# Kernel tuning notes

Hardware: AMD Instinct MI355X
Metric: run time of the kernel (lower is better)

## Reference

```python
import jax, jax.numpy as jnp
import numpy as np

N_NODES = 50000
N_HEDGES = 20000
N_EDGES = 800000
D = 128
H = 4


def setup_inputs() -> dict:
    key = jax.random.key(0)
    ks = jax.random.split(key, 12)
    s = 1.0 / np.sqrt(D)
    return {
        "x_node": jax.random.normal(ks[0], (N_NODES, D), jnp.float32),
        "x_edge": jax.random.normal(ks[1], (N_HEDGES, D), jnp.float32),
        "src": jax.random.randint(ks[2], (N_EDGES,), 0, N_NODES, jnp.int32),
        "dst": jax.random.randint(ks[3], (N_EDGES,), 0, N_HEDGES, jnp.int32),
        "Wq": jax.random.normal(ks[4], (D, D), jnp.float32) * s,
        "bq": jnp.zeros((D,), jnp.float32),
        "Wk": jax.random.normal(ks[5], (D, D), jnp.float32) * s,
        "bk": jnp.zeros((D,), jnp.float32),
        "Wv": jax.random.normal(ks[6], (D, D), jnp.float32) * s,
        "bv": jnp.zeros((D,), jnp.float32),
        "Wo": jax.random.normal(ks[7], (D, D), jnp.float32) * s,
        "bo": jnp.zeros((D,), jnp.float32),
    }


def reference(x_node, x_edge, src, dst, Wq, bq, Wk, bk, Wv, bv, Wo, bo):
    N = x_node.shape[0]
    hd = Wq.shape[1] // H  # head_dim = 32
    Q = (x_node @ Wq + bq).reshape(N, H, hd)
    K = (x_edge @ Wk + bk).reshape(-1, H, hd)
    V = (x_edge @ Wv + bv).reshape(-1, H, hd)
    # per-edge gather: [E, H, hd]
    Qe = Q[src]
    Ke = K[dst]
    Ve = V[dst]
    # per-edge, per-head scores: [E, H]
    scores = jnp.einsum("ehd,ehd->eh", Qe, Ke) / jnp.sqrt(jnp.float32(hd))
    # segment softmax grouped by src node
    m = jax.ops.segment_max(scores, src, num_segments=N)  # [N, H]
    e = jnp.exp(scores - m[src])
    z = jax.ops.segment_sum(e, src, num_segments=N)  # [N, H]
    w = e / z[src]  # [E, H]
    # weighted scatter-add of V messages back to src nodes
    msg = w[:, :, None] * Ve  # [E, H, hd]
    out = jax.ops.segment_sum(msg, src, num_segments=N)  # [N, H, hd]
    out = out.reshape(N, -1)
    return out @ Wo + bo + x_node
```

## Files before the change

### kernel.cpp

```cpp
#include <hip/hip_runtime.h>

#define D 128
#define STRIDE 6144

typedef _Float16 f16;
typedef f16 f16x2 __attribute__((ext_vector_type(2)));
typedef f16 f16x8 __attribute__((ext_vector_type(8)));
typedef float f32x4 __attribute__((ext_vector_type(4)));

__device__ inline f16x2 u2h(unsigned u) { return __builtin_bit_cast(f16x2, u); }
__device__ inline unsigned h2u(f16x2 h) { return __builtin_bit_cast(unsigned, h); }

__device__ inline float dot2(unsigned a, unsigned b, float c) {
#if __has_builtin(__builtin_amdgcn_fdot2)
    return __builtin_amdgcn_fdot2(u2h(a), u2h(b), c, false);
#else
    f16x2 x = u2h(a), y = u2h(b);
    return c + (float)x.x * (float)y.x + (float)x.y * (float)y.y;
#endif
}

__global__ __launch_bounds__(256) void bucket_split(const int* __restrict__ src,
                                                    const int* __restrict__ dst,
                                                    int* __restrict__ bucket_cnt,
                                                    unsigned* __restrict__ temp, int E) {
    __shared__ int hist[256];
    __shared__ int cur[256];
    int t = threadIdx.x;
    hist[t] = 0;
    __syncthreads();
    int base = blockIdx.x * 4096;
    int lim = E - base; if (lim > 4096) lim = 4096;
    for (int i = t; i < lim; i += 256) atomicAdd(&hist[src[base + i] >> 8], 1);
    __syncthreads();
    int h = hist[t];
    if (h) cur[t] = atomicAdd(&bucket_cnt[t], h);
    __syncthreads();
    for (int i = t; i < lim; i += 256) {
        int s = src[base + i];
        int b = s >> 8;
        int pos = atomicAdd(&cur[b], 1);
        if (pos < STRIDE)
            temp[(size_t)b * STRIDE + pos] = ((unsigned)(s & 255) << 24) | (unsigned)dst[base + i];
    }
}

__global__ void bucket_scan(const int* __restrict__ bucket_cnt, int* __restrict__ boff,
                            int* __restrict__ off, int NBUK, int N, int E) {
    __shared__ int sc[256];
    int t = threadIdx.x;
    int v = (t < NBUK) ? bucket_cnt[t] : 0;
    sc[t] = v;
    __syncthreads();
    for (int d0 = 1; d0 < 256; d0 <<= 1) {
        int u = (t >= d0) ? sc[t - d0] : 0;
        __syncthreads();
        sc[t] += u;
        __syncthreads();
    }
    if (t < NBUK) boff[t] = sc[t] - v;
    if (t == 0) { boff[NBUK] = E; off[N] = E; }
}

__global__ __launch_bounds__(256) void bucket_scatter(const unsigned* __restrict__ temp,
                                                      const int* __restrict__ bucket_cnt,
                                                      const int* __restrict__ boff,
                                                      int* __restrict__ off,
                                                      int* __restrict__ csr_dst, int N) {
    __shared__ int nh[256], cur[256], wsum[4];
    __shared__ int lds_dst[STRIDE];
    int b = blockIdx.x, t = threadIdx.x;
    int cnt = bucket_cnt[b];
    if (cnt > STRIDE) cnt = STRIDE;
    int bo = boff[b];
    const unsigned* tb = temp + (size_t)b * STRIDE;
    nh[t] = 0;
    __syncthreads();
    for (int i = t; i < cnt; i += 256) atomicAdd(&nh[tb[i] >> 24], 1);
    __syncthreads();
    int v = nh[t];
    int inc = v;
#pragma unroll
    for (int m = 1; m < 64; m <<= 1) {
        int u = __shfl_up(inc, m);
        if ((t & 63) >= m) inc += u;
    }
    if ((t & 63) == 63) wsum[t >> 6] = inc;
    __syncthreads();
    int add = 0;
#pragma unroll
    for (int w = 0; w < 4; ++w)
        if (w < (t >> 6)) add += wsum[w];
    int ex = add + inc - v;
    cur[t] = ex;
    int node = (b << 8) + t;
    if (node < N) off[node] = bo + ex;
    __syncthreads();
    for (int i = t; i < cnt; i += 256) {
        unsigned it = tb[i];
        int lpos = atomicAdd(&cur[it >> 24], 1);
        lds_dst[lpos] = (int)(it & 0xFFFFFFu);
    }
    __syncthreads();
    for (int i = t; i < cnt; i += 256) csr_dst[bo + i] = lds_dst[i];
}

__global__ void wt_prep4(const float* __restrict__ W0, const float* __restrict__ W1,
                         const float* __restrict__ W2, const float* __restrict__ W3,
                         f16* __restrict__ Wt) {
    const float* W = (blockIdx.x == 0) ? W0 : (blockIdx.x == 1) ? W1 : (blockIdx.x == 2) ? W2 : W3;
    f16* o = Wt + (size_t)blockIdx.x * D * D;
    int t = threadIdx.x;
#pragma unroll
    for (int i = 0; i < 16; ++i) {
        int f = t + i * 256;
        int k = f >> 5, c4 = f & 31;
        float4 v = *(const float4*)(W + k * D + 4 * c4);
        float vv[4] = {v.x, v.y, v.z, v.w};
#pragma unroll
        for (int e = 0; e < 4; ++e) {
            int c = 4 * c4 + e;
            o[c * D + (((k >> 3) ^ (c & 15)) << 3) + (k & 7)] = (f16)vv[e];
        }
    }
}

__device__ inline void stage_w(const f16* __restrict__ Wt, f16* Wl, int t) {
#pragma unroll
    for (int i = 0; i < 8; ++i) ((uint4*)Wl)[t + i * 256] = ((const uint4*)Wt)[t + i * 256];
}

__device__ inline void stage_x_f32(const float* __restrict__ x, f16* xs, int r0, int nrows, int t) {
#pragma unroll
    for (int i = 0; i < 8; ++i) {
        int f = t + i * 256;
        int r = f >> 5, c4 = f & 31;
        int gr = r0 + r;
        float4 v = {0.f, 0.f, 0.f, 0.f};
        if (gr < nrows) v = *(const float4*)(x + (size_t)gr * D + 4 * c4);
        unsigned lo = h2u((f16x2){(f16)v.x, (f16)v.y});
        unsigned hi = h2u((f16x2){(f16)v.z, (f16)v.w});
        *(uint2*)(xs + r * D + (((c4 >> 1) ^ (r & 15)) << 3) + (c4 & 1) * 4) = (uint2){lo, hi};
    }
}

__device__ inline void mfma_core(const f16* xs, const f16* Wl, f32x4 acc[8], int lane, int w) {
    int lr = lane & 15, g = lane >> 4;
    int arow = 16 * w + lr;
#pragma unroll
    for (int kc = 0; kc < 4; ++kc) {
        int slot = kc * 4 + g;
        f16x8 af = *(const f16x8*)(xs + arow * D + ((slot ^ (arow & 15)) << 3));
#pragma unroll
        for (int ct = 0; ct < 8; ++ct) {
            int col = ct * 16 + lr;
            f16x8 bf = *(const f16x8*)(Wl + col * D + ((slot ^ (col & 15)) << 3));
            acc[ct] = __builtin_amdgcn_mfma_f32_16x16x32_f16(af, bf, acc[ct], 0, 0, 0);
        }
    }
}

__global__ __launch_bounds__(256) void gemm_q(const float* __restrict__ x,
                                              const f16* __restrict__ Wt,
                                              const float* __restrict__ b,
                                              f16* __restrict__ y, int nrows, float oscale) {
    __shared__ __align__(16) f16 Wl[D * D];
    __shared__ __align__(16) f16 xs[64 * D];
    int t = threadIdx.x;
    stage_w(Wt, Wl, t);
    int r0 = blockIdx.x * 64;
    stage_x_f32(x, xs, r0, nrows, t);
    __syncthreads();
    int lane = t & 63, w = t >> 6;
    f32x4 acc[8];
#pragma unroll
    for (int i = 0; i < 8; ++i) acc[i] = (f32x4){0.f, 0.f, 0.f, 0.f};
    mfma_core(xs, Wl, acc, lane, w);
    __syncthreads();
    int lr = lane & 15, g = lane >> 4;
#pragma unroll
    for (int ct = 0; ct < 8; ++ct) {
        int col = ct * 16 + lr;
        float bias = b[col];
#pragma unroll
        for (int rg = 0; rg < 4; ++rg) {
            int row = 16 * w + 4 * g + rg;
            xs[row * D + (((col >> 3) ^ (row & 15)) << 3) + (col & 7)] =
                (f16)((acc[ct][rg] + bias) * oscale);
        }
    }
    __syncthreads();
#pragma unroll
    for (int i = 0; i < 4; ++i) {
        int f = t + i * 256;
        int r = f >> 4, c8 = f & 15;
        if (r0 + r < nrows) {
            uint4 v = *(const uint4*)(xs + r * D + ((c8 ^ (r & 15)) << 3));
            *(uint4*)(y + (size_t)(r0 + r) * D + 8 * c8) = v;
        }
    }
}

__global__ __launch_bounds__(256) void gemm_kv(const float* __restrict__ x,
                                               const f16* __restrict__ WtK,
                                               const f16* __restrict__ WtV,
                                               const float* __restrict__ bk,
                                               const float* __restrict__ bv,
                                               f16* __restrict__ y, int nrows) {
    __shared__ __align__(16) f16 Wl[D * D];
    __shared__ __align__(16) f16 xs[64 * D];
    int t = threadIdx.x;
    int r0 = blockIdx.x * 64;
    stage_w(WtK, Wl, t);
    stage_x_f32(x, xs, r0, nrows, t);
    __syncthreads();
    int lane = t & 63, w = t >> 6;
    f32x4 accK[8], accV[8];
#pragma unroll
    for (int i = 0; i < 8; ++i) accK[i] = accV[i] = (f32x4){0.f, 0.f, 0.f, 0.f};
    mfma_core(xs, Wl, accK, lane, w);
    __syncthreads();
    stage_w(WtV, Wl, t);
    __syncthreads();
    mfma_core(xs, Wl, accV, lane, w);
    __syncthreads();
    int lr = lane & 15, g = lane >> 4;
#pragma unroll
    for (int ct = 0; ct < 8; ++ct) {
        int col = ct * 16 + lr;
        float bbk = bk[col], bbv = bv[col];
        int s = col >> 2, wk = col & 3;
#pragma unroll
        for (int rg = 0; rg < 4; ++rg) {
            int row = 16 * w + 4 * g + rg;
            f16* base = Wl + row * 256 + ((s ^ (row & 15)) << 3);
            base[wk] = (f16)(accK[ct][rg] + bbk);
            base[4 + wk] = (f16)(accV[ct][rg] + bbv);
        }
    }
    __syncthreads();
#pragma unroll
    for (int i = 0; i < 8; ++i) {
        int f = t + i * 256;
        int r = f >> 5, c8 = f & 31;
        if (r0 + r < nrows) {
            uint4 v = *(const uint4*)(Wl + r * 256 + ((c8 ^ (r & 15)) << 3));
            *(uint4*)(y + (size_t)(r0 + r) * 256 + 8 * c8) = v;
        }
    }
}

__global__ __launch_bounds__(256) void gemm_o(const f16* __restrict__ aggh,
                                              const f16* __restrict__ Wt,
                                              const float* __restrict__ b,
                                              const float* __restrict__ resid,
                                              float* __restrict__ y, int nrows) {
    __shared__ __align__(16) f16 Wl[D * D];
    __shared__ __align__(16) f16 xs[64 * D];
    int t = threadIdx.x;
    int r0 = blockIdx.x * 64;
    stage_w(Wt, Wl, t);
#pragma unroll
    for (int i = 0; i < 4; ++i) {
        int f = t + i * 256;
        int r = f >> 4, c8 = f & 15;
        int gr = r0 + r;
        uint4 v = {0u, 0u, 0u, 0u};
        if (gr < nrows) v = *(const uint4*)(aggh + (size_t)gr * D + 8 * c8);
        *(uint4*)(xs + r * D + ((c8 ^ (r & 15)) << 3)) = v;
    }
    __syncthreads();
    int lane = t & 63, w = t >> 6;
    f32x4 acc[8];
#pragma unroll
    for (int i = 0; i < 8; ++i) acc[i] = (f32x4){0.f, 0.f, 0.f, 0.f};
    mfma_core(xs, Wl, acc, lane, w);
    __syncthreads();
    float* Tf = (float*)Wl;
    int lr = lane & 15, g = lane >> 4;
#pragma unroll
    for (int ct = 0; ct < 8; ++ct) {
        int col = ct * 16 + lr;
        float bias = b[col];
        int s = col >> 2, wk = col & 3;
#pragma unroll
        for (int rg = 0; rg < 4; ++rg) {
            int row = 16 * w + 4 * g + rg;
            Tf[row * D + ((s ^ (row & 15)) << 2) + wk] = acc[ct][rg] + bias;
        }
    }
    __syncthreads();
#pragma unroll
    for (int i = 0; i < 8; ++i) {
        int f = t + i * 256;
        int r = f >> 5, c4 = f & 31;
        int gr = r0 + r;
        if (gr < nrows) {
            float4 v = *(const float4*)(Tf + r * D + ((c4 ^ (r & 15)) << 2));
            float4 rv = *(const float4*)(resid + (size_t)gr * D + 4 * c4);
            v.x += rv.x; v.y += rv.y; v.z += rv.z; v.w += rv.w;
            *(float4*)(y + (size_t)gr * D + 4 * c4) = v;
        }
    }
}

__global__ void node_attn3(const f16* __restrict__ Qh, const f16* __restrict__ KVh,
                           const int* __restrict__ off, const int* __restrict__ csr,
                           f16* __restrict__ aggh, int N) {
    int wid = (int)((blockIdx.x * (size_t)blockDim.x + threadIdx.x) >> 6);
    int lane = threadIdx.x & 63;
    if (wid >= N) return;
    int j = lane & 15, g = lane >> 4;
    uint4 qu = *(const uint4*)(Qh + (size_t)wid * D + 8 * j);
    int beg = off[wid], end = off[wid + 1];
    float z = 0.f;
    f16x2 a0 = {0, 0}, a1 = {0, 0}, a2 = {0, 0}, a3 = {0, 0};
    if (beg < end) {
        int pe = beg + g;
        int d = csr[(pe < end) ? pe : end - 1];
        for (int p = beg; p < end; p += 4) {
            int pn = p + 4 + g;
            int dn = csr[(pn < end) ? pn : end - 1];
            bool valid = (p + g) < end;
            const f16* row = KVh + (size_t)d * 256 + 16 * j;
            uint4 kv0 = *(const uint4*)row;
            uint4 kv1 = *(const uint4*)(row + 8);
            float s = dot2(kv1.y, qu.w, dot2(kv1.x, qu.z, dot2(kv0.y, qu.y, dot2(kv0.x, qu.x, 0.f))));
            s += __shfl_xor(s, 1);
            s += __shfl_xor(s, 2);
            float eh = valid ? __expf(s) : 0.f;
            z += eh;
            f16 eh16 = (f16)eh;
            f16x2 e2 = {eh16, eh16};
            a0 += e2 * u2h(kv0.z);
            a1 += e2 * u2h(kv0.w);
            a2 += e2 * u2h(kv1.z);
            a3 += e2 * u2h(kv1.w);
            d = dn;
        }
    }
#pragma unroll
    for (int m = 16; m < 64; m <<= 1) {
        z += __shfl_xor(z, m);
        a0 += u2h(__shfl_xor((int)h2u(a0), m));
        a1 += u2h(__shfl_xor((int)h2u(a1), m));
        a2 += u2h(__shfl_xor((int)h2u(a2), m));
        a3 += u2h(__shfl_xor((int)h2u(a3), m));
    }
    if (g == 0) {
        float inv = (end > beg) ? 1.f / z : 0.f;
        uint4 o;
        o.x = h2u((f16x2){(f16)((float)a0.x * inv), (f16)((float)a0.y * inv)});
        o.y = h2u((f16x2){(f16)((float)a1.x * inv), (f16)((float)a1.y * inv)});
        o.z = h2u((f16x2){(f16)((float)a2.x * inv), (f16)((float)a2.y * inv)});
        o.w = h2u((f16x2){(f16)((float)a3.x * inv), (f16)((float)a3.y * inv)});
        *(uint4*)(aggh + (size_t)wid * D + 8 * j) = o;
    }
}

extern "C" void kernel_launch(void* const* d_in, const int* in_sizes, int n_in,
                              void* d_out, int out_size, void* d_ws, size_t ws_size,
                              hipStream_t stream) {
    const float* x_node = (const float*)d_in[0];
    const float* x_edge = (const float*)d_in[1];
    const int* src = (const int*)d_in[2];
    const int* dst = (const int*)d_in[3];
    const float* Wq = (const float*)d_in[4];
    const float* bq = (const float*)d_in[5];
    const float* Wk = (const float*)d_in[6];
    const float* bk = (const float*)d_in[7];
    const float* Wv = (const float*)d_in[8];
    const float* bv = (const float*)d_in[9];
    const float* Wo = (const float*)d_in[10];
    const float* bo = (const float*)d_in[11];

    int N = in_sizes[0] / D;
    int M = in_sizes[1] / D;
    int E = in_sizes[2];
    int NBUK = (N + 255) >> 8;

    char* p = (char*)d_ws;
    auto alloc = [&](size_t bytes) -> char* {
        char* r = p;
        p += (bytes + 15) & ~(size_t)15;
        return r;
    };
    f16* Wt = (f16*)alloc((size_t)4 * D * D * 2);
    f16* Qh = (f16*)alloc((size_t)N * D * 2);
    f16* KVh = (f16*)alloc((size_t)M * 256 * 2);
    f16* aggh = (f16*)alloc((size_t)N * D * 2);
    int* bucket_cnt = (int*)alloc(256 * 4);
    int* boff = (int*)alloc(257 * 4);
    int* off = (int*)alloc((size_t)(N + 1) * 4);
    unsigned* temp = (unsigned*)alloc((size_t)NBUK * STRIDE * 4);
    int* csr_dst = (int*)alloc((size_t)E * 4);
    float* out = (float*)d_out;

    hipMemsetAsync(bucket_cnt, 0, 256 * 4, stream);

    wt_prep4<<<4, 256, 0, stream>>>(Wq, Wk, Wv, Wo, Wt);

    gemm_q<<<(N + 63) / 64, 256, 0, stream>>>(x_node, Wt, bq, Qh, N, 0.17677669529663687f);
    gemm_kv<<<(M + 63) / 64, 256, 0, stream>>>(x_edge, Wt + D * D, Wt + 2 * D * D, bk, bv, KVh, M);

    bucket_split<<<(E + 4095) / 4096, 256, 0, stream>>>(src, dst, bucket_cnt, temp, E);
    bucket_scan<<<1, 256, 0, stream>>>(bucket_cnt, boff, off, NBUK, N, E);
    bucket_scatter<<<NBUK, 256, 0, stream>>>(temp, bucket_cnt, boff, off, csr_dst, N);

    int ablk = (int)(((size_t)N * 64 + 255) / 256);
    node_attn3<<<ablk, 256, 0, stream>>>(Qh, KVh, off, csr_dst, aggh, N);

    gemm_o<<<(N + 63) / 64, 256, 0, stream>>>(aggh, Wt + 3 * D * D, bo, x_node, out, N);
}
```

Baseline: 133.0 us.

## Process eight edges per wave with software-prefetched KV rows in node attention

The node attention kernel now splits each wave into 8 groups of 8 lanes, so 8 edges are handled per iteration instead of 4, and each lane owns 16 feature dims. The K/V row for the next edge is loaded into registers before the current edge is computed, which is meant to hide gather latency. The head reduction needs one fewer shuffle, the final cross-group reduction needs one more step, and register use roughly doubles. Nodes with about 16 edges on average should waste fewer lanes per iteration.

```diff
diff --git a/kernel.cpp b/kernel.cpp
--- a/kernel.cpp
+++ b/kernel.cpp
@@ -304,57 +304,85 @@
     }
 }
 
-__global__ void node_attn3(const f16* __restrict__ Qh, const f16* __restrict__ KVh,
-                           const int* __restrict__ off, const int* __restrict__ csr,
-                           f16* __restrict__ aggh, int N) {
+__global__ __launch_bounds__(256) void node_attn4(const f16* __restrict__ Qh,
+                                                  const f16* __restrict__ KVh,
+                                                  const int* __restrict__ off,
+                                                  const int* __restrict__ csr,
+                                                  f16* __restrict__ aggh, int N) {
     int wid = (int)((blockIdx.x * (size_t)blockDim.x + threadIdx.x) >> 6);
     int lane = threadIdx.x & 63;
     if (wid >= N) return;
-    int j = lane & 15, g = lane >> 4;
-    uint4 qu = *(const uint4*)(Qh + (size_t)wid * D + 8 * j);
+    int j = lane & 7, g = lane >> 3;
+    const f16* qp = Qh + (size_t)wid * D + 16 * j;
+    uint4 qA = *(const uint4*)qp;
+    uint4 qB = *(const uint4*)(qp + 8);
     int beg = off[wid], end = off[wid + 1];
     float z = 0.f;
     f16x2 a0 = {0, 0}, a1 = {0, 0}, a2 = {0, 0}, a3 = {0, 0};
+    f16x2 a4 = {0, 0}, a5 = {0, 0}, a6 = {0, 0}, a7 = {0, 0};
     if (beg < end) {
         int pe = beg + g;
-        int d = csr[(pe < end) ? pe : end - 1];
-        for (int p = beg; p < end; p += 4) {
-            int pn = p + 4 + g;
+        int d0 = csr[(pe < end) ? pe : end - 1];
+        const f16* r = KVh + (size_t)d0 * 256 + 32 * j;
+        uint4 A0 = *(const uint4*)r;
+        uint4 A1 = *(const uint4*)(r + 8);
+        uint4 A2 = *(const uint4*)(r + 16);
+        uint4 A3 = *(const uint4*)(r + 24);
+        for (int p = beg; p < end; p += 8) {
+            int pn = p + 8 + g;
             int dn = csr[(pn < end) ? pn : end - 1];
+            const f16* rn = KVh + (size_t)dn * 256 + 32 * j;
+            uint4 B0 = *(const uint4*)rn;
+            uint4 B1 = *(const uint4*)(rn + 8);
+            uint4 B2 = *(const uint4*)(rn + 16);
+            uint4 B3 = *(const uint4*)(rn + 24);
             bool valid = (p + g) < end;
-            const f16* row = KVh + (size_t)d * 256 + 16 * j;
-            uint4 kv0 = *(const uint4*)row;
-            uint4 kv1 = *(const uint4*)(row + 8);
-            float s = dot2(kv1.y, qu.w, dot2(kv1.x, qu.z, dot2(kv0.y, qu.y, dot2(kv0.x, qu.x, 0.f))));
+            float s = dot2(A0.x, qA.x, 0.f);
+            s = dot2(A0.y, qA.y, s);
+            s = dot2(A1.x, qA.z, s);
+            s = dot2(A1.y, qA.w, s);
+            s = dot2(A2.x, qB.x, s);
+            s = dot2(A2.y, qB.y, s);
+            s = dot2(A3.x, qB.z, s);
+            s = dot2(A3.y, qB.w, s);
             s += __shfl_xor(s, 1);
-            s += __shfl_xor(s, 2);
             float eh = valid ? __expf(s) : 0.f;
             z += eh;
-            f16 eh16 = (f16)eh;
-            f16x2 e2 = {eh16, eh16};
-            a0 += e2 * u2h(kv0.z);
-            a1 += e2 * u2h(kv0.w);
-            a2 += e2 * u2h(kv1.z);
-            a3 += e2 * u2h(kv1.w);
-            d = dn;
-        }
-    }
-#pragma unroll
-    for (int m = 16; m < 64; m <<= 1) {
+            f16 e16 = (f16)eh;
+            f16x2 e2 = {e16, e16};
+            a0 += e2 * u2h(A0.z); a1 += e2 * u2h(A0.w);
+            a2 += e2 * u2h(A1.z); a3 += e2 * u2h(A1.w);
+            a4 += e2 * u2h(A2.z); a5 += e2 * u2h(A2.w);
+            a6 += e2 * u2h(A3.z); a7 += e2 * u2h(A3.w);
+            A0 = B0; A1 = B1; A2 = B2; A3 = B3;
+        }
+    }
+#pragma unroll
+    for (int m = 8; m < 64; m <<= 1) {
         z += __shfl_xor(z, m);
         a0 += u2h(__shfl_xor((int)h2u(a0), m));
         a1 += u2h(__shfl_xor((int)h2u(a1), m));
         a2 += u2h(__shfl_xor((int)h2u(a2), m));
         a3 += u2h(__shfl_xor((int)h2u(a3), m));
+        a4 += u2h(__shfl_xor((int)h2u(a4), m));
+        a5 += u2h(__shfl_xor((int)h2u(a5), m));
+        a6 += u2h(__shfl_xor((int)h2u(a6), m));
+        a7 += u2h(__shfl_xor((int)h2u(a7), m));
     }
     if (g == 0) {
         float inv = (end > beg) ? 1.f / z : 0.f;
-        uint4 o;
-        o.x = h2u((f16x2){(f16)((float)a0.x * inv), (f16)((float)a0.y * inv)});
-        o.y = h2u((f16x2){(f16)((float)a1.x * inv), (f16)((float)a1.y * inv)});
-        o.z = h2u((f16x2){(f16)((float)a2.x * inv), (f16)((float)a2.y * inv)});
-        o.w = h2u((f16x2){(f16)((float)a3.x * inv), (f16)((float)a3.y * inv)});
-        *(uint4*)(aggh + (size_t)wid * D + 8 * j) = o;
+        uint4 o0, o1;
+        o0.x = h2u((f16x2){(f16)((float)a0.x * inv), (f16)((float)a0.y * inv)});
+        o0.y = h2u((f16x2){(f16)((float)a1.x * inv), (f16)((float)a1.y * inv)});
+        o0.z = h2u((f16x2){(f16)((float)a2.x * inv), (f16)((float)a2.y * inv)});
+        o0.w = h2u((f16x2){(f16)((float)a3.x * inv), (f16)((float)a3.y * inv)});
+        o1.x = h2u((f16x2){(f16)((float)a4.x * inv), (f16)((float)a4.y * inv)});
+        o1.y = h2u((f16x2){(f16)((float)a5.x * inv), (f16)((float)a5.y * inv)});
+        o1.z = h2u((f16x2){(f16)((float)a6.x * inv), (f16)((float)a6.y * inv)});
+        o1.w = h2u((f16x2){(f16)((float)a7.x * inv), (f16)((float)a7.y * inv)});
+        f16* op = aggh + (size_t)wid * D + 16 * j;
+        *(uint4*)op = o0;
+        *(uint4*)(op + 8) = o1;
     }
 }
 
@@ -408,7 +436,7 @@
     bucket_scatter<<<NBUK, 256, 0, stream>>>(temp, bucket_cnt, boff, off, csr_dst, N);
 
     int ablk = (int)(((size_t)N * 64 + 255) / 256);
-    node_attn3<<<ablk, 256, 0, stream>>>(Qh, KVh, off, csr_dst, aggh, N);
+    node_attn4<<<ablk, 256, 0, stream>>>(Qh, KVh, off, csr_dst, aggh, N);
 
     gemm_o<<<(N + 63) / 64, 256, 0, stream>>>(aggh, Wt + 3 * D * D, bo, x_node, out, N);
 }
```

Result: no change. 131.0 us (-1.5%).
